# Kernel tuning notes

Hardware: AMD Instinct MI355X
Metric: run time of the kernel (lower is better)

The kernel has to match this reference:

```python
import jax, jax.numpy as jnp
import numpy as np

B, QL, T, H = 32, 1, 2048, 512


def setup_inputs() -> dict:
    key = jax.random.key(0)
    ks = jax.random.split(key, 10)
    n = lambda i, shape, sc=1.0: jax.random.normal(ks[i], shape, dtype=jnp.float32) * sc
    inv = 1.0 / np.sqrt(H)
    return {
        "query": n(0, (B, QL, H)),
        "value": n(1, (B, T, H)),
        "last_attn": jax.random.uniform(ks[2], (B, T), dtype=jnp.float32),
        "conv_w": n(3, (H, 1, 3), 0.1),   # Conv1d weight (out_ch, in_ch=1, k=3)
        "conv_b": n(4, (H,), 0.1),
        "q_w": n(5, (H, H), inv),          # query_proj (no bias)
        "v_w": n(6, (H, H), inv),          # value_proj (no bias)
        "s_w": n(7, (1, H), inv),          # score_proj weight
        "s_b": n(8, (1,), 0.1),            # score_proj bias
        "bias": n(9, (H,), 0.1),           # learned additive bias
    }


def reference(query, value, last_attn, conv_w, conv_b, q_w, v_w, s_w, s_b, bias):
    Tlen = last_attn.shape[1]
    # Conv1d(in=1, out=H, k=3, pad=1) over last_attn, then transpose -> (B, T, H)
    pad = jnp.pad(last_attn, ((0, 0), (1, 1)))
    frames = jnp.stack([pad[:, k:k + Tlen] for k in range(3)], axis=0)  # (3, B, T)
    conv_attn = jnp.einsum('hk,kbt->bth', conv_w[:, 0, :], frames) + conv_b  # (B, T, H)
    q = jnp.einsum('bqh,oh->bqo', query, q_w)   # (B, 1, H)
    v = jnp.einsum('bth,oh->bto', value, v_w)   # (B, T, H)
    e = jnp.tanh(q + v + conv_attn + bias)      # (B, T, H), q broadcasts over T
    score = jnp.einsum('bth,oh->bt', e, s_w) + s_b  # (B, T)
    # smoothing=True branch: sigmoid then L1-normalize
    score = jax.nn.sigmoid(score)
    attn = score / jnp.sum(score, axis=-1, keepdims=True)
    context = jnp.einsum('bt,bth->bh', attn, value)  # bmm(attn[:,None,:], value).squeeze(1)
    return context, attn
```

## Files before the change

kernel.cpp:

```cpp
#include <hip/hip_runtime.h>
#include <math.h>

#define B 32
#define T 2048
#define H 512

#define BT2 64
#define APAD 40

typedef __attribute__((ext_vector_type(8))) __bf16 bf16x8;
typedef __attribute__((ext_vector_type(4))) __bf16 bf16x4v;
typedef __attribute__((ext_vector_type(4))) float f32x4;
typedef __attribute__((ext_vector_type(4))) float floatx4;

union pack8 { bf16x4v h; uint2 u; };

static __device__ __forceinline__ void gl_lds16(const void* g, void* l) {
    __builtin_amdgcn_global_load_lds(
        (const __attribute__((address_space(1))) void*)g,
        (__attribute__((address_space(3))) void*)l, 16, 0, 0);
}

__global__ __launch_bounds__(256) void k_init(const float* __restrict__ query,
                                              const float* __restrict__ q_w,
                                              const float* __restrict__ bias,
                                              const float* __restrict__ v_w,
                                              float* __restrict__ qpb,
                                              unsigned short* __restrict__ wbf,
                                              float* __restrict__ ctx_num,
                                              float* __restrict__ denom) {
    const int blk = blockIdx.x;
    const int tid = threadIdx.x;

    if (blk >= 288) {
#pragma unroll
        for (int i = 0; i < 16; ++i) {
            const int off = tid * 4 + i * 1024;
            *(f32x4*)(ctx_num + off) = (f32x4){0.f, 0.f, 0.f, 0.f};
        }
        if (tid < B) denom[tid] = 0.f;
        return;
    }
    if (blk >= 256) {
        const int c = blk - 256;
        const size_t base = (size_t)c * 8192 + tid * 4;
#pragma unroll
        for (int i = 0; i < 8; ++i) {
            const size_t off = base + (size_t)i * 1024;
            f32x4 a = *(const f32x4*)(v_w + off);
            pack8 p;
            p.h = __builtin_convertvector(a, bf16x4v);
            *(uint2*)(wbf + off) = p.u;
        }
        return;
    }

    const int b = blk >> 3;
    const int s = blk & 7;
    const int wave = tid >> 6;
    const int lane = tid & 63;

    const float* qb = query + (size_t)b * H + lane * 8;
    float4 q0 = *(const float4*)qb;
    float4 q1 = *(const float4*)(qb + 4);

    const int o0 = s * 64 + wave * 16;
#pragma unroll
    for (int i = 0; i < 16; ++i) {
        const int o = o0 + i;
        const float* wr = q_w + (size_t)o * H + lane * 8;
        float4 w0 = *(const float4*)wr;
        float4 w1 = *(const float4*)(wr + 4);
        float acc = w0.x * q0.x + w0.y * q0.y + w0.z * q0.z + w0.w * q0.w +
                    w1.x * q1.x + w1.y * q1.y + w1.z * q1.z + w1.w * q1.w;
#pragma unroll
        for (int m = 1; m < 64; m <<= 1) acc += __shfl_xor(acc, m);
        if (lane == 0) qpb[b * H + o] = acc + bias[o];
    }
}

__global__ __launch_bounds__(512, 4) void k2_fused(const float* __restrict__ value,
                                                   const unsigned short* __restrict__ wbf,
                                                   const float* __restrict__ la,
                                                   const float* __restrict__ conv_w,
                                                   const float* __restrict__ conv_b,
                                                   const float* __restrict__ s_w,
                                                   const float* __restrict__ qpb,
                                                   const float* __restrict__ s_b,
                                                   float* __restrict__ pre_sg,
                                                   float* __restrict__ ctx_num,
                                                   float* __restrict__ denom) {
    __shared__ __align__(16) unsigned short As[BT2 * APAD];
    __shared__ __align__(16) unsigned short Bs[H * 32];
    __shared__ float las[BT2 + 2];
    __shared__ float redp[BT2][9];
    __shared__ float sgs[BT2];

    const int t0 = blockIdx.x * BT2;
    const int b  = blockIdx.y;
    const int tid = threadIdx.x;
    const int wave = tid >> 6;
    const int lane = tid & 63;
    const int tx   = lane & 15;
    const int quad = lane >> 4;
    const int wn   = wave * 64;

    if (tid < BT2 + 2) {
        const int t = t0 + tid - 1;
        las[tid] = (t >= 0 && t < T) ? la[b * T + t] : 0.f;
    }

    float qp4[4], sw4[4], cb4[4], c04[4], c14[4], c24[4];
#pragma unroll
    for (int ni = 0; ni < 4; ++ni) {
        const int ol = wn + ni * 16 + tx;
        qp4[ni] = qpb[b * H + ol];
        sw4[ni] = s_w[ol];
        cb4[ni] = conv_b[ol];
        c04[ni] = conv_w[ol * 3 + 0];
        c14[ni] = conv_w[ol * 3 + 1];
        c24[ni] = conv_w[ol * 3 + 2];
    }

    floatx4 acc[4][4];
#pragma unroll
    for (int i = 0; i < 4; ++i)
#pragma unroll
        for (int j = 0; j < 4; ++j) acc[i][j] = (floatx4){0.f, 0.f, 0.f, 0.f};

    const int arow = tid >> 3;
    const int acol = (tid & 7) * 4;
    const float* agp = value + ((size_t)b * T + t0 + arow) * H + acol;
    const int brow = lane >> 2;
    const int bcol = (lane & 3) * 8;
    const unsigned short* gB[4];
    unsigned short* lB[4];
#pragma unroll
    for (int c = 0; c < 4; ++c) {
        const int chunk = wave + c * 8;
        gB[c] = wbf + (size_t)(chunk * 16 + brow) * H + bcol;
        lB[c] = &Bs[chunk * 512];
    }

    for (int kc = 0; kc < H; kc += 32) {
        f32x4 av = *(const f32x4*)(agp + kc);

        __syncthreads();
#pragma unroll
        for (int c = 0; c < 4; ++c) gl_lds16(gB[c] + kc, lB[c]);

        pack8 p;
        p.h = __builtin_convertvector(av, bf16x4v);
        *(uint2*)&As[arow * APAD + acol] = p.u;

        __syncthreads();

        bf16x8 af[4], bfr[4];
#pragma unroll
        for (int mi = 0; mi < 4; ++mi)
            af[mi] = *(const bf16x8*)&As[(mi * 16 + tx) * APAD + quad * 8];
#pragma unroll
        for (int ni = 0; ni < 4; ++ni)
            bfr[ni] = *(const bf16x8*)&Bs[(wn + ni * 16 + tx) * 32 + quad * 8];
#pragma unroll
        for (int mi = 0; mi < 4; ++mi)
#pragma unroll
            for (int ni = 0; ni < 4; ++ni)
                acc[mi][ni] = __builtin_amdgcn_mfma_f32_16x16x32_bf16(
                    af[mi], bfr[ni], acc[mi][ni], 0, 0, 0);
    }

    float sacc[16];
#pragma unroll
    for (int i = 0; i < 16; ++i) sacc[i] = 0.f;
#pragma unroll
    for (int ni = 0; ni < 4; ++ni) {
#pragma unroll
        for (int mi = 0; mi < 4; ++mi)
#pragma unroll
            for (int r = 0; r < 4; ++r) {
                const int tl = mi * 16 + quad * 4 + r;
                const float conv = c04[ni] * las[tl] + c14[ni] * las[tl + 1] +
                                   c24[ni] * las[tl + 2] + cb4[ni];
                const float x = acc[mi][ni][r] + qp4[ni] + conv;
                const float ex = __expf(2.f * x);
                const float th = 1.f - 2.f * __builtin_amdgcn_rcpf(ex + 1.f);
                sacc[mi * 4 + r] += sw4[ni] * th;
            }
    }
#pragma unroll
    for (int i = 0; i < 16; ++i) {
        float v = sacc[i];
        v += __shfl_xor(v, 1);
        v += __shfl_xor(v, 2);
        v += __shfl_xor(v, 4);
        v += __shfl_xor(v, 8);
        if (tx == 0) redp[(i >> 2) * 16 + quad * 4 + (i & 3)][wave] = v;
    }
    __syncthreads();

    if (tid < BT2) {
        float sc = s_b[0];
#pragma unroll
        for (int w = 0; w < 8; ++w) sc += redp[tid][w];
        const float sg = 1.f / (1.f + __expf(-sc));
        sgs[tid] = sg;
        pre_sg[b * T + t0 + tid] = sg;
        float dsum = sg;
#pragma unroll
        for (int m = 1; m < 64; m <<= 1) dsum += __shfl_xor(dsum, m);
        if (tid == 0) atomicAdd(&denom[b], dsum);
    }
    __syncthreads();

    float* redc = (float*)Bs;
    const int h4 = (tid & 127) * 4;
    const int tp = tid >> 7;
    f32x4 a = {0.f, 0.f, 0.f, 0.f};
    const float* vb = value + ((size_t)b * T + t0) * H + h4;
    for (int t = tp; t < BT2; t += 4) {
        const float w = sgs[t];
        f32x4 v = *(const f32x4*)(vb + (size_t)t * H);
        a.x += w * v.x; a.y += w * v.y; a.z += w * v.z; a.w += w * v.w;
    }
    *(f32x4*)&redc[tp * 512 + h4] = a;
    __syncthreads();
    if (tid < 128) {
        const int h = tid * 4;
        f32x4 r0 = *(const f32x4*)&redc[0 * 512 + h];
        f32x4 r1 = *(const f32x4*)&redc[1 * 512 + h];
        f32x4 r2 = *(const f32x4*)&redc[2 * 512 + h];
        f32x4 r3 = *(const f32x4*)&redc[3 * 512 + h];
        atomicAdd(&ctx_num[b * H + h + 0], r0.x + r1.x + r2.x + r3.x);
        atomicAdd(&ctx_num[b * H + h + 1], r0.y + r1.y + r2.y + r3.y);
        atomicAdd(&ctx_num[b * H + h + 2], r0.z + r1.z + r2.z + r3.z);
        atomicAdd(&ctx_num[b * H + h + 3], r0.w + r1.w + r2.w + r3.w);
    }
}

__global__ __launch_bounds__(256) void k3_scale(const float* __restrict__ pre_sg,
                                                const float* __restrict__ ctx_num,
                                                const float* __restrict__ denom,
                                                float* __restrict__ attn_out,
                                                float* __restrict__ ctx) {
    const int b = blockIdx.x;
    const int tid = threadIdx.x;
    const float inv = 1.f / denom[b];
#pragma unroll
    for (int i = 0; i < 8; ++i) {
        const int t = tid + i * 256;
        attn_out[b * T + t] = pre_sg[b * T + t] * inv;
    }
#pragma unroll
    for (int i = 0; i < 2; ++i) {
        const int h = tid + i * 256;
        ctx[b * H + h] = ctx_num[b * H + h] * inv;
    }
}

extern "C" void kernel_launch(void* const* d_in, const int* in_sizes, int n_in,
                              void* d_out, int out_size, void* d_ws, size_t ws_size,
                              hipStream_t stream) {
    const float* query  = (const float*)d_in[0];
    const float* value  = (const float*)d_in[1];
    const float* la     = (const float*)d_in[2];
    const float* conv_w = (const float*)d_in[3];
    const float* conv_b = (const float*)d_in[4];
    const float* q_w    = (const float*)d_in[5];
    const float* v_w    = (const float*)d_in[6];
    const float* s_w    = (const float*)d_in[7];
    const float* s_b    = (const float*)d_in[8];
    const float* bias   = (const float*)d_in[9];

    float* out  = (float*)d_out;
    float* ctx  = out;
    float* attn = out + B * H;

    float* qpb     = (float*)d_ws;
    float* pre_sg  = qpb + B * H;
    float* ctx_num = pre_sg + B * T;
    float* denom   = ctx_num + B * H;
    unsigned short* wbf = (unsigned short*)(denom + 64);

    k_init<<<289, 256, 0, stream>>>(query, q_w, bias, v_w, qpb, wbf, ctx_num, denom);

    dim3 g2(T / BT2, B);
    k2_fused<<<g2, 512, 0, stream>>>(value, wbf, la, conv_w, conv_b, s_w, qpb, s_b,
                                     pre_sg, ctx_num, denom);

    k3_scale<<<B, 256, 0, stream>>>(pre_sg, ctx_num, denom, attn, ctx);
}
```

Before: 279.3 us.

## Double-buffer LDS tiles and prefetch value rows in the GEMM mainloop

```diff
diff --git a/kernel.cpp b/kernel.cpp
--- a/kernel.cpp
+++ b/kernel.cpp
@@ -90,8 +90,8 @@
                                                    float* __restrict__ pre_sg,
                                                    float* __restrict__ ctx_num,
                                                    float* __restrict__ denom) {
-    __shared__ __align__(16) unsigned short As[BT2 * APAD];
-    __shared__ __align__(16) unsigned short Bs[H * 32];
+    __shared__ __align__(16) unsigned short As[2][BT2 * APAD];
+    __shared__ __align__(16) unsigned short Bs[2][H * 32];
     __shared__ float las[BT2 + 2];
     __shared__ float redp[BT2][9];
     __shared__ float sgs[BT2];
@@ -110,6 +110,73 @@
         las[tid] = (t >= 0 && t < T) ? la[b * T + t] : 0.f;
     }
 
+    floatx4 acc[4][4];
+#pragma unroll
+    for (int i = 0; i < 4; ++i)
+#pragma unroll
+        for (int j = 0; j < 4; ++j) acc[i][j] = (floatx4){0.f, 0.f, 0.f, 0.f};
+
+    const int arow = tid >> 3;
+    const int acol = (tid & 7) * 4;
+    const float* agp = value + ((size_t)b * T + t0 + arow) * H + acol;
+
+    const int brow = lane >> 2;
+    const int bcs  = ((lane & 3) ^ ((lane >> 3) & 3)) * 8;
+    const unsigned short* gB = wbf + (size_t)(wave * 16 + brow) * H + bcs;
+    const int rsw = (tx >> 1) & 3;
+
+    {
+#pragma unroll
+        for (int c = 0; c < 4; ++c)
+            gl_lds16(gB + (size_t)c * 128 * H, &Bs[0][(wave + c * 8) * 512]);
+        f32x4 a0 = *(const f32x4*)agp;
+        pack8 p;
+        p.h = __builtin_convertvector(a0, bf16x4v);
+        *(uint2*)&As[0][arow * APAD + acol] = p.u;
+    }
+    f32x4 avW = *(const f32x4*)(agp + 32);
+    f32x4 avP = *(const f32x4*)(agp + 64);
+    __syncthreads();
+
+#pragma unroll 2
+    for (int t = 0; t < 16; ++t) {
+        const int buf = t & 1;
+
+        if (t < 15) {
+#pragma unroll
+            for (int c = 0; c < 4; ++c)
+                gl_lds16(gB + (size_t)c * 128 * H + (t + 1) * 32,
+                         &Bs[buf ^ 1][(wave + c * 8) * 512]);
+        }
+        f32x4 avN = (f32x4){0.f, 0.f, 0.f, 0.f};
+        if (t < 13) avN = *(const f32x4*)(agp + (t + 3) * 32);
+
+        bf16x8 af[4], bfr[4];
+#pragma unroll
+        for (int mi = 0; mi < 4; ++mi)
+            af[mi] = *(const bf16x8*)&As[buf][(mi * 16 + tx) * APAD + quad * 8];
+#pragma unroll
+        for (int ni = 0; ni < 4; ++ni)
+            bfr[ni] = *(const bf16x8*)&Bs[buf][(wn + ni * 16 + tx) * 32 + ((quad ^ rsw) << 3)];
+
+        if (t < 15) {
+            pack8 p;
+            p.h = __builtin_convertvector(avW, bf16x4v);
+            *(uint2*)&As[buf ^ 1][arow * APAD + acol] = p.u;
+            avW = avP;
+            avP = avN;
+        }
+
+#pragma unroll
+        for (int mi = 0; mi < 4; ++mi)
+#pragma unroll
+            for (int ni = 0; ni < 4; ++ni)
+                acc[mi][ni] = __builtin_amdgcn_mfma_f32_16x16x32_bf16(
+                    af[mi], bfr[ni], acc[mi][ni], 0, 0, 0);
+
+        if (t < 15) __syncthreads();
+    }
+
     float qp4[4], sw4[4], cb4[4], c04[4], c14[4], c24[4];
 #pragma unroll
     for (int ni = 0; ni < 4; ++ni) {
@@ -120,54 +187,6 @@
         c04[ni] = conv_w[ol * 3 + 0];
         c14[ni] = conv_w[ol * 3 + 1];
         c24[ni] = conv_w[ol * 3 + 2];
-    }
-
-    floatx4 acc[4][4];
-#pragma unroll
-    for (int i = 0; i < 4; ++i)
-#pragma unroll
-        for (int j = 0; j < 4; ++j) acc[i][j] = (floatx4){0.f, 0.f, 0.f, 0.f};
-
-    const int arow = tid >> 3;
-    const int acol = (tid & 7) * 4;
-    const float* agp = value + ((size_t)b * T + t0 + arow) * H + acol;
-    const int brow = lane >> 2;
-    const int bcol = (lane & 3) * 8;
-    const unsigned short* gB[4];
-    unsigned short* lB[4];
-#pragma unroll
-    for (int c = 0; c < 4; ++c) {
-        const int chunk = wave + c * 8;
-        gB[c] = wbf + (size_t)(chunk * 16 + brow) * H + bcol;
-        lB[c] = &Bs[chunk * 512];
-    }
-
-    for (int kc = 0; kc < H; kc += 32) {
-        f32x4 av = *(const f32x4*)(agp + kc);
-
-        __syncthreads();
-#pragma unroll
-        for (int c = 0; c < 4; ++c) gl_lds16(gB[c] + kc, lB[c]);
-
-        pack8 p;
-        p.h = __builtin_convertvector(av, bf16x4v);
-        *(uint2*)&As[arow * APAD + acol] = p.u;
-
-        __syncthreads();
-
-        bf16x8 af[4], bfr[4];
-#pragma unroll
-        for (int mi = 0; mi < 4; ++mi)
-            af[mi] = *(const bf16x8*)&As[(mi * 16 + tx) * APAD + quad * 8];
-#pragma unroll
-        for (int ni = 0; ni < 4; ++ni)
-            bfr[ni] = *(const bf16x8*)&Bs[(wn + ni * 16 + tx) * 32 + quad * 8];
-#pragma unroll
-        for (int mi = 0; mi < 4; ++mi)
-#pragma unroll
-            for (int ni = 0; ni < 4; ++ni)
-                acc[mi][ni] = __builtin_amdgcn_mfma_f32_16x16x32_bf16(
-                    af[mi], bfr[ni], acc[mi][ni], 0, 0, 0);
     }
 
     float sacc[16];
```

Result: slower. 292.7 us (+4.8%).

## Stage whole value tile in LDS and stream pre-swizzled weights from global

Applied to the files above, without the earlier changes.

```diff
diff --git a/kernel.cpp b/kernel.cpp
--- a/kernel.cpp
+++ b/kernel.cpp
@@ -5,8 +5,8 @@
 #define T 2048
 #define H 512
 
-#define BT2 64
-#define APAD 40
+#define BT2 32
+#define ASTR 520
 
 typedef __attribute__((ext_vector_type(8))) __bf16 bf16x8;
 typedef __attribute__((ext_vector_type(4))) __bf16 bf16x4v;
@@ -14,12 +14,6 @@
 typedef __attribute__((ext_vector_type(4))) float floatx4;
 
 union pack8 { bf16x4v h; uint2 u; };
-
-static __device__ __forceinline__ void gl_lds16(const void* g, void* l) {
-    __builtin_amdgcn_global_load_lds(
-        (const __attribute__((address_space(1))) void*)g,
-        (__attribute__((address_space(3))) void*)l, 16, 0, 0);
-}
 
 __global__ __launch_bounds__(256) void k_init(const float* __restrict__ query,
                                               const float* __restrict__ q_w,
@@ -42,15 +36,22 @@
         return;
     }
     if (blk >= 256) {
-        const int c = blk - 256;
-        const size_t base = (size_t)c * 8192 + tid * 4;
-#pragma unroll
-        for (int i = 0; i < 8; ++i) {
-            const size_t off = base + (size_t)i * 1024;
-            f32x4 a = *(const f32x4*)(v_w + off);
-            pack8 p;
-            p.h = __builtin_convertvector(a, bf16x4v);
-            *(uint2*)(wbf + off) = p.u;
+        const int c2 = blk - 256;
+        const int wv = tid >> 6;
+        const int lane = tid & 63;
+        const int srow = (c2 >> 2) * 64 + (c2 & 3) * 16 + (lane & 15);
+        const int scol0 = (lane >> 4) * 8;
+#pragma unroll
+        for (int kk = 0; kk < 4; ++kk) {
+            const int k = wv * 4 + kk;
+            const float* src = v_w + (size_t)srow * H + k * 32 + scol0;
+            f32x4 a0 = *(const f32x4*)src;
+            f32x4 a1 = *(const f32x4*)(src + 4);
+            pack8 p0, p1;
+            p0.h = __builtin_convertvector(a0, bf16x4v);
+            p1.h = __builtin_convertvector(a1, bf16x4v);
+            uint4 u = {p0.u.x, p0.u.y, p1.u.x, p1.u.y};
+            *(uint4*)(wbf + ((size_t)c2 * 16 + k) * 512 + lane * 8) = u;
         }
         return;
     }
@@ -90,8 +91,7 @@
                                                    float* __restrict__ pre_sg,
                                                    float* __restrict__ ctx_num,
                                                    float* __restrict__ denom) {
-    __shared__ __align__(16) unsigned short As[BT2 * APAD];
-    __shared__ __align__(16) unsigned short Bs[H * 32];
+    __shared__ __align__(16) unsigned short As[BT2 * ASTR];
     __shared__ float las[BT2 + 2];
     __shared__ float redp[BT2][9];
     __shared__ float sgs[BT2];
@@ -110,6 +110,51 @@
         las[tid] = (t >= 0 && t < T) ? la[b * T + t] : 0.f;
     }
 
+    {
+        const int srow = tid >> 4;
+        const int scol = (tid & 15) * 8;
+        const float* sg = value + ((size_t)b * T + t0 + srow) * H + scol;
+        unsigned short* sl = &As[srow * ASTR + scol];
+#pragma unroll
+        for (int c = 0; c < 4; ++c) {
+            f32x4 a0 = *(const f32x4*)(sg + c * 128);
+            f32x4 a1 = *(const f32x4*)(sg + c * 128 + 4);
+            pack8 p0, p1;
+            p0.h = __builtin_convertvector(a0, bf16x4v);
+            p1.h = __builtin_convertvector(a1, bf16x4v);
+            uint4 u = {p0.u.x, p0.u.y, p1.u.x, p1.u.y};
+            *(uint4*)(sl + c * 128) = u;
+        }
+    }
+    __syncthreads();
+
+    floatx4 acc[2][4];
+#pragma unroll
+    for (int i = 0; i < 2; ++i)
+#pragma unroll
+        for (int j = 0; j < 4; ++j) acc[i][j] = (floatx4){0.f, 0.f, 0.f, 0.f};
+
+    const unsigned short* gB = wbf + (size_t)wave * 32768 + lane * 8;
+    const unsigned short* aB = &As[tx * ASTR + quad * 8];
+
+#pragma unroll 4
+    for (int k = 0; k < 16; ++k) {
+        bf16x8 bfr[4];
+#pragma unroll
+        for (int ni = 0; ni < 4; ++ni)
+            bfr[ni] = *(const bf16x8*)(gB + ni * 8192 + k * 512);
+        bf16x8 af[2];
+#pragma unroll
+        for (int mi = 0; mi < 2; ++mi)
+            af[mi] = *(const bf16x8*)(aB + mi * 16 * ASTR + k * 32);
+#pragma unroll
+        for (int mi = 0; mi < 2; ++mi)
+#pragma unroll
+            for (int ni = 0; ni < 4; ++ni)
+                acc[mi][ni] = __builtin_amdgcn_mfma_f32_16x16x32_bf16(
+                    af[mi], bfr[ni], acc[mi][ni], 0, 0, 0);
+    }
+
     float qp4[4], sw4[4], cb4[4], c04[4], c14[4], c24[4];
 #pragma unroll
     for (int ni = 0; ni < 4; ++ni) {
@@ -122,61 +167,13 @@
         c24[ni] = conv_w[ol * 3 + 2];
     }
 
-    floatx4 acc[4][4];
-#pragma unroll
-    for (int i = 0; i < 4; ++i)
-#pragma unroll
-        for (int j = 0; j < 4; ++j) acc[i][j] = (floatx4){0.f, 0.f, 0.f, 0.f};
-
-    const int arow = tid >> 3;
-    const int acol = (tid & 7) * 4;
-    const float* agp = value + ((size_t)b * T + t0 + arow) * H + acol;
-    const int brow = lane >> 2;
-    const int bcol = (lane & 3) * 8;
-    const unsigned short* gB[4];
-    unsigned short* lB[4];
-#pragma unroll
-    for (int c = 0; c < 4; ++c) {
-        const int chunk = wave + c * 8;
-        gB[c] = wbf + (size_t)(chunk * 16 + brow) * H + bcol;
-        lB[c] = &Bs[chunk * 512];
-    }
-
-    for (int kc = 0; kc < H; kc += 32) {
-        f32x4 av = *(const f32x4*)(agp + kc);
-
-        __syncthreads();
-#pragma unroll
-        for (int c = 0; c < 4; ++c) gl_lds16(gB[c] + kc, lB[c]);
-
-        pack8 p;
-        p.h = __builtin_convertvector(av, bf16x4v);
-        *(uint2*)&As[arow * APAD + acol] = p.u;
-
-        __syncthreads();
-
-        bf16x8 af[4], bfr[4];
-#pragma unroll
-        for (int mi = 0; mi < 4; ++mi)
-            af[mi] = *(const bf16x8*)&As[(mi * 16 + tx) * APAD + quad * 8];
-#pragma unroll
-        for (int ni = 0; ni < 4; ++ni)
-            bfr[ni] = *(const bf16x8*)&Bs[(wn + ni * 16 + tx) * 32 + quad * 8];
-#pragma unroll
-        for (int mi = 0; mi < 4; ++mi)
-#pragma unroll
-            for (int ni = 0; ni < 4; ++ni)
-                acc[mi][ni] = __builtin_amdgcn_mfma_f32_16x16x32_bf16(
-                    af[mi], bfr[ni], acc[mi][ni], 0, 0, 0);
-    }
-
-    float sacc[16];
-#pragma unroll
-    for (int i = 0; i < 16; ++i) sacc[i] = 0.f;
+    float sacc[8];
+#pragma unroll
+    for (int i = 0; i < 8; ++i) sacc[i] = 0.f;
 #pragma unroll
     for (int ni = 0; ni < 4; ++ni) {
 #pragma unroll
-        for (int mi = 0; mi < 4; ++mi)
+        for (int mi = 0; mi < 2; ++mi)
 #pragma unroll
             for (int r = 0; r < 4; ++r) {
                 const int tl = mi * 16 + quad * 4 + r;
@@ -189,7 +186,7 @@
             }
     }
 #pragma unroll
-    for (int i = 0; i < 16; ++i) {
+    for (int i = 0; i < 8; ++i) {
         float v = sacc[i];
         v += __shfl_xor(v, 1);
         v += __shfl_xor(v, 2);
@@ -208,12 +205,12 @@
         pre_sg[b * T + t0 + tid] = sg;
         float dsum = sg;
 #pragma unroll
-        for (int m = 1; m < 64; m <<= 1) dsum += __shfl_xor(dsum, m);
+        for (int m = 1; m < 32; m <<= 1) dsum += __shfl_xor(dsum, m);
         if (tid == 0) atomicAdd(&denom[b], dsum);
     }
     __syncthreads();
 
-    float* redc = (float*)Bs;
+    float* redc = (float*)As;
     const int h4 = (tid & 127) * 4;
     const int tp = tid >> 7;
     f32x4 a = {0.f, 0.f, 0.f, 0.f};
```

Result: no change. 275.0 us (-1.5%).
